# Optimization experiments

Measured on AMD Instinct MI355X. Metric: run time of the kernel, lower is better.

## Reference

```python
import jax, jax.numpy as jnp
import numpy as np

N = 200000
D = 128
B = 8
VS = 0.4
XMIN, YMIN, ZMIN = -50.0, -50.0, -5.0
NX, NY, NZ = 250, 250, 20
VXYZ = NX * NY * NZ
FILL = np.int32(2_000_000_000)  # > any real voxel key, so padded uniques sort last
BN_EPS = 1e-5


def _bn(x, g, b, m, v):
    # BatchNorm1d in eval mode with given running stats
    return (x - m) * jax.lax.rsqrt(v + BN_EPS) * g + b


def _leaky(x):
    return jnp.where(x >= 0, x, 0.1 * x)


def setup_inputs() -> dict:
    key = jax.random.key(0)
    ks = jax.random.split(key, 12)
    points_feature = jax.random.normal(ks[0], (N, D), jnp.float32)
    u = jax.random.uniform(ks[1], (N, 3), jnp.float32)
    lo = jnp.array([XMIN, YMIN, ZMIN], jnp.float32)
    ext = jnp.array([100.0, 100.0, 8.0], jnp.float32)
    points_center = lo + 0.001 + u * (ext - 0.002)  # strictly inside pc_range
    batch_idx = jax.random.randint(ks[2], (N,), 0, B, jnp.int32)
    foreground_mask = jax.random.randint(ks[3], (N,), 0, 2, jnp.int32).astype(bool)
    timestamp = jax.random.normal(ks[4], (B,), jnp.float32) * 0.1
    w_pf = jax.random.normal(ks[5], (3 * D, D), jnp.float32) / np.sqrt(3 * D)
    b_pf = jax.random.normal(ks[6], (D,), jnp.float32) * 0.01
    g_pf = jax.random.uniform(ks[7], (D,), jnp.float32) + 0.5
    be_pf = jax.random.normal(ks[8], (D,), jnp.float32) * 0.1
    m_pf = jax.random.normal(ks[9], (D,), jnp.float32) * 0.1
    v_pf = jax.random.uniform(ks[10], (D,), jnp.float32) + 0.5
    ks2 = jax.random.split(ks[11], 6)
    w_cp = jax.random.normal(ks2[0], (D, D), jnp.float32) / np.sqrt(D)
    b_cp = jax.random.normal(ks2[1], (D,), jnp.float32) * 0.01
    g_cp = jax.random.uniform(ks2[2], (D,), jnp.float32) + 0.5
    be_cp = jax.random.normal(ks2[3], (D,), jnp.float32) * 0.1
    m_cp = jax.random.normal(ks2[4], (D,), jnp.float32) * 0.1
    v_cp = jax.random.uniform(ks2[5], (D,), jnp.float32) + 0.5
    return dict(points_feature=points_feature, points_center=points_center,
                batch_idx=batch_idx, foreground_mask=foreground_mask,
                timestamp=timestamp,
                w_pf=w_pf, b_pf=b_pf, g_pf=g_pf, be_pf=be_pf, m_pf=m_pf, v_pf=v_pf,
                w_cp=w_cp, b_cp=b_cp, g_cp=g_cp, be_cp=be_cp, m_cp=m_cp, v_cp=v_cp)


def reference(points_feature, points_center, batch_idx, foreground_mask, timestamp,
              w_pf, b_pf, g_pf, be_pf, m_pf, v_pf,
              w_cp, b_cp, g_cp, be_cp, m_cp, v_cp):
    # NOTE: the original forward computes a time position embedding and then
    # overwrites it with zeros_like, so its net contribution is exactly zero.
    n = points_feature.shape[0]
    # voxelize point centers -> (b, xi, yi, zi) encoded as a single int key
    xi = jnp.floor((points_center[:, 0] - XMIN) / VS).astype(jnp.int32)
    yi = jnp.floor((points_center[:, 1] - YMIN) / VS).astype(jnp.int32)
    zi = jnp.floor((points_center[:, 2] - ZMIN) / VS).astype(jnp.int32)
    vkey = ((batch_idx.astype(jnp.int32) * NX + xi) * NY + yi) * NZ + zi
    # torch.unique(dim=0) sorts lexicographically == sorted scalar keys
    uk, inv = jnp.unique(vkey, return_inverse=True, size=n, fill_value=FILL)
    fgf = foreground_mask.astype(points_feature.dtype)
    # K = points_cluster_idx_fore.max() + 1 (number of foreground clusters)
    K = jnp.max(jnp.where(foreground_mask, inv, -1)) + 1
    # scatter_mean of foreground point features per cluster (empty -> 0)
    cnt = jax.ops.segment_sum(fgf, inv, num_segments=n)
    csum = jax.ops.segment_sum(points_feature * fgf[:, None], inv, num_segments=n)
    cmean = csum / jnp.maximum(cnt, 1.0)[:, None]
    proj = _leaky(_bn(cmean @ w_cp + b_cp, g_cp, be_cp, m_cp, v_cp))
    valid = jnp.arange(n) < K
    # cluster_feature_all: rows < K hold projected cluster features, rest are 0
    cfa = jnp.where(valid[:, None], proj, 0.0)
    # associate voxels: halve the batch id (agent pairing), re-unique
    akey = (uk // VXYZ // 2) * VXYZ + uk % VXYZ
    _, ainv = jnp.unique(akey, return_inverse=True, size=n, fill_value=FILL)
    # scatter_mean of cluster features over associate voxels (only valid clusters)
    acnt = jax.ops.segment_sum(valid.astype(points_feature.dtype), ainv, num_segments=n)
    asum = jax.ops.segment_sum(cfa, ainv, num_segments=n)
    amean = asum / jnp.maximum(acnt, 1.0)[:, None]
    pf_assoc = amean[ainv[inv]]   # gather per point via voxel -> associate id
    pf_clu = cfa[inv]             # gather per point cluster feature
    amask = (pf_clu - pf_assoc).sum(axis=1) > 0
    cat = jnp.concatenate([points_feature, pf_clu, pf_assoc], axis=1)
    h = _leaky(_bn(cat @ w_pf + b_pf, g_pf, be_pf, m_pf, v_pf))
    newf = jnp.where(amask[:, None], h, points_feature)
    # original early-returns points_feature if associate_mask.sum() <= 1
    return jnp.where(amask.sum() > 1, newf, points_feature)
```

## Files before the change

### kernel.cpp

```cpp
#include <hip/hip_runtime.h>

#define SCAN_BS 256
#define SCAN_IT 16
#define SCAN_CHUNK (SCAN_BS * SCAN_IT)
#define NVOX 10000000
#define NAVOX 5000000
#define NWORDS1 312500
#define NWORDS2 156250
#define VXYZK 1250000

__device__ __forceinline__ float leakyf(float x) { return x >= 0.0f ? x : 0.1f * x; }

__device__ __forceinline__ int fg_get(const void* fgp, int i, int mode) {
  return mode ? (((const unsigned char*)fgp)[i] != 0) : (((const int*)fgp)[i] != 0);
}

__global__ void k_vkey(const float* __restrict__ pc, const int* __restrict__ bidx,
                       const unsigned* __restrict__ fgw, int nw,
                       int* __restrict__ vkey, unsigned* __restrict__ bits,
                       int* __restrict__ c, int N) {
  int i = blockIdx.x * blockDim.x + threadIdx.x;
  if (i < nw && fgw[i] > 1u) atomicOr(&c[4], 1);
  if (i >= N) return;
  float x = pc[3 * i], y = pc[3 * i + 1], z = pc[3 * i + 2];
  int xi = (int)floorf((x - (-50.0f)) / 0.4f);
  int yi = (int)floorf((y - (-50.0f)) / 0.4f);
  int zi = (int)floorf((z - (-5.0f)) / 0.4f);
  xi = min(max(xi, 0), 249); yi = min(max(yi, 0), 249); zi = min(max(zi, 0), 19);
  int b = min(max(bidx[i], 0), 7);
  int key = ((b * 250 + xi) * 250 + yi) * 20 + zi;
  vkey[i] = key;
  atomicOr(&bits[key >> 5], 1u << (key & 31));
}

__global__ void k_scan_pop(const unsigned* __restrict__ bits, int nwords,
                           unsigned* __restrict__ wordpfx, unsigned* __restrict__ bsums) {
  __shared__ unsigned s[SCAN_BS];
  int tid = threadIdx.x;
  long base = (long)blockIdx.x * SCAN_CHUNK + (long)tid * SCAN_IT;
  unsigned v[SCAN_IT];
  unsigned tsum = 0;
#pragma unroll
  for (int j = 0; j < SCAN_IT; ++j) {
    long idx = base + j;
    v[j] = (idx < (long)nwords) ? (unsigned)__popc(bits[idx]) : 0u;
    tsum += v[j];
  }
  unsigned x = tsum;
  s[tid] = x;
  for (int off = 1; off < SCAN_BS; off <<= 1) {
    __syncthreads();
    unsigned y = (tid >= off) ? s[tid - off] : 0u;
    __syncthreads();
    x += y;
    s[tid] = x;
  }
  if (tid == SCAN_BS - 1) bsums[blockIdx.x] = x;
  unsigned run = x - tsum;
#pragma unroll
  for (int j = 0; j < SCAN_IT; ++j) {
    long idx = base + j;
    if (idx < (long)nwords) { wordpfx[idx] = run; run += v[j]; }
  }
}

__global__ void k_scan_sums(unsigned* __restrict__ data, int n, int* __restrict__ totalOut) {
  __shared__ unsigned s[SCAN_BS];
  int tid = threadIdx.x;
  int base = tid * SCAN_IT;
  unsigned v[SCAN_IT];
  unsigned tsum = 0;
#pragma unroll
  for (int j = 0; j < SCAN_IT; ++j) {
    int idx = base + j;
    v[j] = (idx < n) ? data[idx] : 0u;
    tsum += v[j];
  }
  unsigned x = tsum;
  s[tid] = x;
  for (int off = 1; off < SCAN_BS; off <<= 1) {
    __syncthreads();
    unsigned y = (tid >= off) ? s[tid - off] : 0u;
    __syncthreads();
    x += y;
    s[tid] = x;
  }
  if (tid == SCAN_BS - 1) *totalOut = (int)x;
  unsigned run = x - tsum;
#pragma unroll
  for (int j = 0; j < SCAN_IT; ++j) {
    int idx = base + j;
    if (idx < n) { data[idx] = run; run += v[j]; }
  }
}

__device__ __forceinline__ int rank_of(int key, const unsigned* bits,
                                       const unsigned* wordpfx, const unsigned* bsums) {
  int w = key >> 5, b = key & 31;
  return (int)(wordpfx[w] + bsums[w >> 12] + (unsigned)__popc(bits[w] & ((1u << b) - 1u)));
}

__global__ void k_inv_ukey(const int* __restrict__ vkey, const unsigned* __restrict__ bits,
                           const unsigned* __restrict__ wordpfx, const unsigned* __restrict__ bsums,
                           const void* __restrict__ fgp, int* __restrict__ inv,
                           int* __restrict__ ukey, int* __restrict__ c, int N) {
  int i = blockIdx.x * blockDim.x + threadIdx.x;
  bool valid = i < N;
  int mode = c[4];
  int r = 0;
  if (valid) {
    int k = vkey[i];
    r = rank_of(k, bits, wordpfx, bsums);
    inv[i] = r;
    ukey[r] = k;
  }
  int fgr = (valid && fg_get(fgp, i, mode)) ? r : -1;
  for (int off = 32; off > 0; off >>= 1) fgr = max(fgr, __shfl_down(fgr, off));
  if ((threadIdx.x & 63) == 0 && fgr >= 0) atomicMax(&c[2], fgr + 1);
}

__global__ void k_akey_mark(const int* __restrict__ ukey, int* __restrict__ akey,
                            unsigned* __restrict__ abits, const int* __restrict__ c, int N) {
  int r = blockIdx.x * blockDim.x + threadIdx.x;
  if (r >= N || r >= c[0]) return;
  int uk = ukey[r];
  int ak = (uk / VXYZK / 2) * VXYZK + uk % VXYZK;
  akey[r] = ak;
  atomicOr(&abits[ak >> 5], 1u << (ak & 31));
}

__global__ void k_ainv(const int* __restrict__ akey, const unsigned* __restrict__ abits,
                       const unsigned* __restrict__ awordpfx, const unsigned* __restrict__ bsums,
                       int* __restrict__ ainv, unsigned* __restrict__ gcnt,
                       const int* __restrict__ c, int N) {
  int r = blockIdx.x * blockDim.x + threadIdx.x;
  if (r >= N || r >= c[0]) return;
  int g = rank_of(akey[r], abits, awordpfx, bsums);
  ainv[r] = g;
  atomicAdd(&gcnt[g], 1u);
}

__global__ void k_build_lists(const int* __restrict__ ainv_u, const unsigned* __restrict__ gcnt,
                              int* __restrict__ mlist, int* __restrict__ nlist,
                              unsigned char* __restrict__ needp, int* __restrict__ c, int N) {
  int r = blockIdx.x * blockDim.x + threadIdx.x;
  if (r >= N || r >= c[0]) return;
  if (gcnt[ainv_u[r]] >= 2u) {
    int mp = atomicAdd(&c[5], 1);
    mlist[mp] = r;
    if (r < c[2]) {
      needp[r] = 1;
      int np = atomicAdd(&c[6], 1);
      nlist[np] = r;
    }
  }
}

__global__ void k_zero_filter(const int* __restrict__ mlist, const int* __restrict__ ainv_u,
                              const void* __restrict__ fgp, const int* __restrict__ inv,
                              const unsigned char* __restrict__ needp,
                              float* __restrict__ csum, float* __restrict__ asum,
                              float* __restrict__ cnt, int* __restrict__ clist,
                              int* __restrict__ c, int N) {
  int stride = gridDim.x * blockDim.x;
  int tid0 = blockIdx.x * blockDim.x + threadIdx.x;
  int K = c[2];
  int totalA = c[5] * 128;
  for (int idx = tid0; idx < totalA; idx += stride) {
    int r = mlist[idx >> 7];
    int d = idx & 127;
    asum[(size_t)ainv_u[r] * 128 + d] = 0.0f;
    if (r < K) csum[(size_t)r * 128 + d] = 0.0f;
  }
  int mode = c[4];
  for (int i = tid0; i < N; i += stride) {
    if (!fg_get(fgp, i, mode)) continue;
    int r = inv[i];
    if (!needp[r]) continue;
    atomicAdd(&cnt[r], 1.0f);
    int p = atomicAdd(&c[7], 1);
    clist[p] = i;
  }
}

__global__ void k_csum_accum(const float* __restrict__ pf, const int* __restrict__ clist,
                             const int* __restrict__ inv, float* __restrict__ csum,
                             const int* __restrict__ c) {
  int total = c[7] * 128;
  int stride = gridDim.x * blockDim.x;
  for (int idx = blockIdx.x * blockDim.x + threadIdx.x; idx < total; idx += stride) {
    int i = clist[idx >> 7];
    int d = idx & 127;
    atomicAdd(&csum[(size_t)inv[i] * 128 + d], pf[(size_t)i * 128 + d]);
  }
}

__global__ __launch_bounds__(128) void k_proj16(
    float* __restrict__ cs, const float* __restrict__ cnt, const int* __restrict__ nlist,
    const float* __restrict__ W, const float* __restrict__ bb,
    const float* __restrict__ gg, const float* __restrict__ be,
    const float* __restrict__ mm, const float* __restrict__ vv, const int* __restrict__ c) {
  int nc = c[6];
  int ntiles = (nc + 15) >> 4;
  __shared__ __align__(16) float tile[16][128];
  __shared__ int srow[16];
  int d = threadIdx.x;
  for (int tb = blockIdx.x; tb < ntiles; tb += gridDim.x) {
    int base = tb * 16;
    if (d < 16) srow[d] = (base + d < nc) ? nlist[base + d] : -1;
    __syncthreads();
    for (int p = 0; p < 16; ++p) {
      int r = srow[p];
      tile[p][d] = (r >= 0) ? cs[(size_t)r * 128 + d] / fmaxf(cnt[r], 1.0f) : 0.0f;
    }
    __syncthreads();
    float acc[16];
#pragma unroll
    for (int p = 0; p < 16; ++p) acc[p] = 0.0f;
    for (int k4 = 0; k4 < 32; ++k4) {
      float w0 = W[(4 * k4 + 0) * 128 + d];
      float w1 = W[(4 * k4 + 1) * 128 + d];
      float w2 = W[(4 * k4 + 2) * 128 + d];
      float w3 = W[(4 * k4 + 3) * 128 + d];
#pragma unroll
      for (int p = 0; p < 16; ++p) {
        float4 t4 = *(const float4*)&tile[p][4 * k4];
        acc[p] = fmaf(t4.x, w0, acc[p]);
        acc[p] = fmaf(t4.y, w1, acc[p]);
        acc[p] = fmaf(t4.z, w2, acc[p]);
        acc[p] = fmaf(t4.w, w3, acc[p]);
      }
    }
    float biasd = bb[d], scale = gg[d] / sqrtf(vv[d] + 1e-5f), md = mm[d], bed = be[d];
    for (int p = 0; p < 16; ++p) {
      int r = srow[p];
      if (r >= 0) {
        float pre = acc[p] + biasd;
        cs[(size_t)r * 128 + d] = leakyf((pre - md) * scale + bed);
      }
    }
    __syncthreads();
  }
}

__global__ void k_asum_accum(const float* __restrict__ cs, const int* __restrict__ nlist,
                             const int* __restrict__ ainv_u, float* __restrict__ asum,
                             float* __restrict__ acnt, const int* __restrict__ c) {
  int total = c[6] * 128;
  int stride = gridDim.x * blockDim.x;
  for (int idx = blockIdx.x * blockDim.x + threadIdx.x; idx < total; idx += stride) {
    int r = nlist[idx >> 7];
    int d = idx & 127;
    int g = ainv_u[r];
    atomicAdd(&asum[(size_t)g * 128 + d], cs[(size_t)r * 128 + d]);
    if (d == 0) atomicAdd(&acnt[g], 1.0f);
  }
}

__global__ void k_amask2(const float* __restrict__ cs, const float* __restrict__ asum,
                         const float* __restrict__ acnt, const int* __restrict__ ainv_u,
                         const int* __restrict__ mlist, const int* __restrict__ c,
                         unsigned* __restrict__ flag) {
  int mcount = c[5];
  int groups = gridDim.x * (blockDim.x >> 6);
  int j0 = blockIdx.x * (blockDim.x >> 6) + (threadIdx.x >> 6);
  int lane = threadIdx.x & 63;
  int K = c[2];
  for (int j = j0; j < mcount; j += groups) {
    int r = mlist[j];
    int g = ainv_u[r];
    float mc = fmaxf(acnt[g], 1.0f);
    bool valid = r < K;
    size_t rb = (size_t)r * 128, gb = (size_t)g * 128;
    float c0 = valid ? cs[rb + lane] : 0.0f;
    float c1 = valid ? cs[rb + 64 + lane] : 0.0f;
    float s = (c0 - asum[gb + lane] / mc) + (c1 - asum[gb + 64 + lane] / mc);
    for (int off = 32; off > 0; off >>= 1) s += __shfl_down(s, off);
    if (lane == 0) flag[r] = (s > 0.0f) ? 1u : 0u;
  }
}

__global__ void k_plist(const int* __restrict__ inv, const unsigned* __restrict__ flag,
                        int* __restrict__ plist, int* __restrict__ c, int N) {
  int i = blockIdx.x * blockDim.x + threadIdx.x;
  bool pred = (i < N) && (flag[inv[i]] != 0u);
  unsigned long long m = __ballot(pred);
  int lane = threadIdx.x & 63;
  int cnt = __popcll(m);
  int base = 0;
  if (lane == 0 && cnt) base = atomicAdd(&c[3], cnt);
  base = __shfl(base, 0);
  if (pred) plist[base + __popcll(m & ((1ull << lane) - 1ull))] = i;
}

__global__ __launch_bounds__(128) void k_fgemm(
    const float* __restrict__ pf, const float* __restrict__ cs,
    const float* __restrict__ asum, const float* __restrict__ acnt,
    const int* __restrict__ inv, const int* __restrict__ ainv_u,
    const int* __restrict__ plist, const int* __restrict__ c,
    const float* __restrict__ W, const float* __restrict__ bb,
    const float* __restrict__ gg, const float* __restrict__ be,
    const float* __restrict__ mm, const float* __restrict__ vv,
    float* __restrict__ out) {
  int pcnt = c[3];
  if (pcnt <= 1) return;
  int K = c[2];
  int ntiles = (pcnt + 15) >> 4;
  __shared__ __align__(16) float tile[16][384];
  __shared__ int si[16], sr[16], sg[16];
  __shared__ float smc[16];
  int t = threadIdx.x;
  for (int tb = blockIdx.x; tb < ntiles; tb += gridDim.x) {
    int base = tb * 16;
    if (t < 16) {
      int i = (base + t < pcnt) ? plist[base + t] : -1;
      si[t] = i;
      int r = (i >= 0) ? inv[i] : 0;
      sr[t] = r;
      int g = ainv_u[r];
      sg[t] = g;
      smc[t] = fmaxf(acnt[g], 1.0f);
    }
    __syncthreads();
    for (int e = t; e < 16 * 96; e += 128) {
      int p = e / 96, f4 = e % 96;
      int i = si[p];
      float4 v = make_float4(0.f, 0.f, 0.f, 0.f);
      if (i >= 0) {
        if (f4 < 32) {
          v = ((const float4*)pf)[(size_t)i * 32 + f4];
        } else if (f4 < 64) {
          int r = sr[p];
          if (r < K) v = ((const float4*)cs)[(size_t)r * 32 + (f4 - 32)];
        } else {
          float4 a = ((const float4*)asum)[(size_t)sg[p] * 32 + (f4 - 64)];
          float mc = smc[p];
          v = make_float4(a.x / mc, a.y / mc, a.z / mc, a.w / mc);
        }
      }
      *(float4*)&tile[p][f4 * 4] = v;
    }
    __syncthreads();
    float acc[16];
#pragma unroll
    for (int p = 0; p < 16; ++p) acc[p] = 0.0f;
    for (int k4 = 0; k4 < 96; ++k4) {
      float w0 = W[(4 * k4 + 0) * 128 + t];
      float w1 = W[(4 * k4 + 1) * 128 + t];
      float w2 = W[(4 * k4 + 2) * 128 + t];
      float w3 = W[(4 * k4 + 3) * 128 + t];
#pragma unroll
      for (int p = 0; p < 16; ++p) {
        float4 t4 = *(const float4*)&tile[p][4 * k4];
        acc[p] = fmaf(t4.x, w0, acc[p]);
        acc[p] = fmaf(t4.y, w1, acc[p]);
        acc[p] = fmaf(t4.z, w2, acc[p]);
        acc[p] = fmaf(t4.w, w3, acc[p]);
      }
    }
    float biasd = bb[t], scale = gg[t] / sqrtf(vv[t] + 1e-5f), md = mm[t], bed = be[t];
    for (int p = 0; p < 16; ++p) {
      int i = si[p];
      if (i >= 0) {
        float pre = acc[p] + biasd;
        out[(size_t)i * 128 + t] = leakyf((pre - md) * scale + bed);
      }
    }
    __syncthreads();
  }
}

extern "C" void kernel_launch(void* const* d_in, const int* in_sizes, int n_in,
                              void* d_out, int out_size, void* d_ws, size_t ws_size,
                              hipStream_t stream) {
  (void)n_in; (void)out_size; (void)ws_size;
  const float* pf   = (const float*)d_in[0];
  const float* pc   = (const float*)d_in[1];
  const int*   bidx = (const int*)d_in[2];
  const void*  fgp  = d_in[3];
  const float* Wpf  = (const float*)d_in[5];
  const float* bpf  = (const float*)d_in[6];
  const float* gpf  = (const float*)d_in[7];
  const float* bepf = (const float*)d_in[8];
  const float* mpf  = (const float*)d_in[9];
  const float* vpf  = (const float*)d_in[10];
  const float* Wcp  = (const float*)d_in[11];
  const float* bcp  = (const float*)d_in[12];
  const float* gcp  = (const float*)d_in[13];
  const float* becp = (const float*)d_in[14];
  const float* mcp  = (const float*)d_in[15];
  const float* vcp  = (const float*)d_in[16];
  float* out = (float*)d_out;
  int N = in_sizes[0] / 128;

  char* ws = (char*)d_ws;
  size_t o = 0;
  auto take = [&](size_t bytes) -> void* {
    void* p = ws + o;
    o += (bytes + 255) & ~(size_t)255;
    return p;
  };
  unsigned* bits   = (unsigned*)take((size_t)NWORDS1 * 4);
  unsigned* abits  = (unsigned*)take((size_t)NWORDS2 * 4);
  float* cnt       = (float*)take((size_t)N * 4);
  float* acnt      = (float*)take((size_t)N * 4);
  unsigned* flag   = (unsigned*)take((size_t)N * 4);
  unsigned* gcnt   = (unsigned*)take((size_t)N * 4);
  unsigned char* needp = (unsigned char*)take((size_t)N);
  int* ctr         = (int*)take(256);
  size_t zeroBytes = o;
  unsigned* wordpfx  = (unsigned*)take((size_t)NWORDS1 * 4);
  unsigned* awordpfx = (unsigned*)take((size_t)NWORDS2 * 4);
  unsigned* bsums1 = (unsigned*)take((size_t)4096 * 4);
  unsigned* bsums2 = (unsigned*)take((size_t)4096 * 4);
  int* vkey        = (int*)take((size_t)N * 4);
  int* inv         = (int*)take((size_t)N * 4);
  int* ukey        = (int*)take((size_t)N * 4);
  int* akey        = (int*)take((size_t)N * 4);
  int* ainv_u      = (int*)take((size_t)N * 4);
  int* nlist       = (int*)take((size_t)N * 4);
  int* clist       = (int*)take((size_t)N * 4);
  float* csum      = (float*)take((size_t)N * 128 * 4);
  float* asum      = (float*)take((size_t)N * 128 * 4);
  int* mlist = vkey;
  int* plist = akey;

  hipMemcpyAsync(out, pf, (size_t)N * 128 * sizeof(float),
                 hipMemcpyDeviceToDevice, stream);

  hipMemsetAsync(ws, 0, zeroBytes, stream);

  int nb = (N + 255) / 256;
  int nw = N / 4;
  k_vkey<<<nb, 256, 0, stream>>>(pc, bidx, (const unsigned*)fgp, nw, vkey, bits, ctr, N);

  int blk1 = (NWORDS1 + SCAN_CHUNK - 1) / SCAN_CHUNK;
  k_scan_pop<<<blk1, SCAN_BS, 0, stream>>>(bits, NWORDS1, wordpfx, bsums1);
  k_scan_sums<<<1, SCAN_BS, 0, stream>>>(bsums1, blk1, &ctr[0]);
  k_inv_ukey<<<nb, 256, 0, stream>>>(vkey, bits, wordpfx, bsums1, fgp, inv, ukey, ctr, N);

  k_akey_mark<<<nb, 256, 0, stream>>>(ukey, akey, abits, ctr, N);
  int blk2 = (NWORDS2 + SCAN_CHUNK - 1) / SCAN_CHUNK;
  k_scan_pop<<<blk2, SCAN_BS, 0, stream>>>(abits, NWORDS2, awordpfx, bsums2);
  k_scan_sums<<<1, SCAN_BS, 0, stream>>>(bsums2, blk2, &ctr[1]);
  k_ainv<<<nb, 256, 0, stream>>>(akey, abits, awordpfx, bsums2, ainv_u, gcnt, ctr, N);

  k_build_lists<<<nb, 256, 0, stream>>>(ainv_u, gcnt, mlist, nlist, needp, ctr, N);
  k_zero_filter<<<1024, 256, 0, stream>>>(mlist, ainv_u, fgp, inv, needp,
                                          csum, asum, cnt, clist, ctr, N);
  k_csum_accum<<<1024, 256, 0, stream>>>(pf, clist, inv, csum, ctr);
  k_proj16<<<512, 128, 0, stream>>>(csum, cnt, nlist, Wcp, bcp, gcp, becp, mcp, vcp, ctr);
  k_asum_accum<<<512, 256, 0, stream>>>(csum, nlist, ainv_u, asum, acnt, ctr);
  k_amask2<<<512, 256, 0, stream>>>(csum, asum, acnt, ainv_u, mlist, ctr, flag);

  k_plist<<<nb, 256, 0, stream>>>(inv, flag, plist, ctr, N);
  k_fgemm<<<1024, 128, 0, stream>>>(pf, csum, asum, acnt, inv, ainv_u, plist, ctr,
                                    Wpf, bpf, gpf, bepf, mpf, vpf, out);
}
```

Measured before the change: 467.6 us.

## Fuse output copy into voxel-key kernel and merge akey and asum passes

The device-to-device memcpy of the point features into the output moves into the voxel-key kernel as a grid-stride float4 copy. The associate-key marking is folded into the inverse-rank kernel, computed per point rather than per unique voxel, which drops the ukey buffer and one launch. The asum/acnt scatter is fused into the cluster projection epilogue, removing a separate kernel and a re-read of csum. In exchange, the abits atomics now run once per point instead of once per unique voxel, and the output copy no longer uses the copy engine.

```diff
diff --git a/kernel.cpp b/kernel.cpp
--- a/kernel.cpp
+++ b/kernel.cpp
@@ -8,6 +8,8 @@
 #define NWORDS1 312500
 #define NWORDS2 156250
 #define VXYZK 1250000
+#define BLK1 ((NWORDS1 + SCAN_CHUNK - 1) / SCAN_CHUNK)
+#define BLK2 ((NWORDS2 + SCAN_CHUNK - 1) / SCAN_CHUNK)
 
 __device__ __forceinline__ float leakyf(float x) { return x >= 0.0f ? x : 0.1f * x; }
 
@@ -15,22 +17,40 @@
   return mode ? (((const unsigned char*)fgp)[i] != 0) : (((const int*)fgp)[i] != 0);
 }
 
-__global__ void k_vkey(const float* __restrict__ pc, const int* __restrict__ bidx,
-                       const unsigned* __restrict__ fgw, int nw,
-                       int* __restrict__ vkey, unsigned* __restrict__ bits,
-                       int* __restrict__ c, int N) {
-  int i = blockIdx.x * blockDim.x + threadIdx.x;
-  if (i < nw && fgw[i] > 1u) atomicOr(&c[4], 1);
-  if (i >= N) return;
-  float x = pc[3 * i], y = pc[3 * i + 1], z = pc[3 * i + 2];
-  int xi = (int)floorf((x - (-50.0f)) / 0.4f);
-  int yi = (int)floorf((y - (-50.0f)) / 0.4f);
-  int zi = (int)floorf((z - (-5.0f)) / 0.4f);
-  xi = min(max(xi, 0), 249); yi = min(max(yi, 0), 249); zi = min(max(zi, 0), 19);
-  int b = min(max(bidx[i], 0), 7);
-  int key = ((b * 250 + xi) * 250 + yi) * 20 + zi;
-  vkey[i] = key;
-  atomicOr(&bits[key >> 5], 1u << (key & 31));
+__device__ __forceinline__ int rank_of(int key, const unsigned* bits,
+                                       const unsigned* wordpfx, const unsigned* bsums) {
+  int w = key >> 5, b = key & 31;
+  return (int)(wordpfx[w] + bsums[w >> 12] + (unsigned)__popc(bits[w] & ((1u << b) - 1u)));
+}
+
+__global__ void k_vkey_copy(const float* __restrict__ pc, const int* __restrict__ bidx,
+                            const unsigned* __restrict__ fgw, int nw,
+                            int* __restrict__ vkey, unsigned* __restrict__ bits,
+                            int* __restrict__ c, const float* __restrict__ pf,
+                            float* __restrict__ out, int N) {
+  int nth = gridDim.x * blockDim.x;
+  int gtid = blockIdx.x * blockDim.x + threadIdx.x;
+  for (int i = gtid; i < N; i += nth) {
+    if (i < nw && fgw[i] > 1u) atomicOr(&c[4], 1);
+    float x = pc[3 * i], y = pc[3 * i + 1], z = pc[3 * i + 2];
+    int xi = (int)floorf((x - (-50.0f)) / 0.4f);
+    int yi = (int)floorf((y - (-50.0f)) / 0.4f);
+    int zi = (int)floorf((z - (-5.0f)) / 0.4f);
+    xi = min(max(xi, 0), 249); yi = min(max(yi, 0), 249); zi = min(max(zi, 0), 19);
+    int b = min(max(bidx[i], 0), 7);
+    int key = ((b * 250 + xi) * 250 + yi) * 20 + zi;
+    vkey[i] = key;
+    atomicOr(&bits[key >> 5], 1u << (key & 31));
+  }
+  const float4* s4 = (const float4*)pf;
+  float4* d4 = (float4*)out;
+  int n4 = N * 32;
+  int e = gtid;
+  for (; e + 3 * nth < n4; e += 4 * nth) {
+    float4 v0 = s4[e], v1 = s4[e + nth], v2 = s4[e + 2 * nth], v3 = s4[e + 3 * nth];
+    d4[e] = v0; d4[e + nth] = v1; d4[e + 2 * nth] = v2; d4[e + 3 * nth] = v3;
+  }
+  for (; e < n4; e += nth) d4[e] = s4[e];
 }
 
 __global__ void k_scan_pop(const unsigned* __restrict__ bits, int nwords,
@@ -94,16 +114,11 @@
   }
 }
 
-__device__ __forceinline__ int rank_of(int key, const unsigned* bits,
-                                       const unsigned* wordpfx, const unsigned* bsums) {
-  int w = key >> 5, b = key & 31;
-  return (int)(wordpfx[w] + bsums[w >> 12] + (unsigned)__popc(bits[w] & ((1u << b) - 1u)));
-}
-
-__global__ void k_inv_ukey(const int* __restrict__ vkey, const unsigned* __restrict__ bits,
+__global__ void k_inv_akey(const int* __restrict__ vkey, const unsigned* __restrict__ bits,
                            const unsigned* __restrict__ wordpfx, const unsigned* __restrict__ bsums,
                            const void* __restrict__ fgp, int* __restrict__ inv,
-                           int* __restrict__ ukey, int* __restrict__ c, int N) {
+                           int* __restrict__ akey, unsigned* __restrict__ abits,
+                           int* __restrict__ c, int N) {
   int i = blockIdx.x * blockDim.x + threadIdx.x;
   bool valid = i < N;
   int mode = c[4];
@@ -112,21 +127,13 @@
     int k = vkey[i];
     r = rank_of(k, bits, wordpfx, bsums);
     inv[i] = r;
-    ukey[r] = k;
+    int ak = (k / VXYZK / 2) * VXYZK + k % VXYZK;
+    akey[r] = ak;
+    atomicOr(&abits[ak >> 5], 1u << (ak & 31));
   }
   int fgr = (valid && fg_get(fgp, i, mode)) ? r : -1;
   for (int off = 32; off > 0; off >>= 1) fgr = max(fgr, __shfl_down(fgr, off));
   if ((threadIdx.x & 63) == 0 && fgr >= 0) atomicMax(&c[2], fgr + 1);
-}
-
-__global__ void k_akey_mark(const int* __restrict__ ukey, int* __restrict__ akey,
-                            unsigned* __restrict__ abits, const int* __restrict__ c, int N) {
-  int r = blockIdx.x * blockDim.x + threadIdx.x;
-  if (r >= N || r >= c[0]) return;
-  int uk = ukey[r];
-  int ak = (uk / VXYZK / 2) * VXYZK + uk % VXYZK;
-  akey[r] = ak;
-  atomicOr(&abits[ak >> 5], 1u << (ak & 31));
 }
 
 __global__ void k_ainv(const int* __restrict__ akey, const unsigned* __restrict__ abits,
@@ -195,8 +202,9 @@
   }
 }
 
-__global__ __launch_bounds__(128) void k_proj16(
+__global__ __launch_bounds__(128) void k_proj_asum(
     float* __restrict__ cs, const float* __restrict__ cnt, const int* __restrict__ nlist,
+    const int* __restrict__ ainv_u, float* __restrict__ asum, float* __restrict__ acnt,
     const float* __restrict__ W, const float* __restrict__ bb,
     const float* __restrict__ gg, const float* __restrict__ be,
     const float* __restrict__ mm, const float* __restrict__ vv, const int* __restrict__ c) {
@@ -236,24 +244,14 @@
       int r = srow[p];
       if (r >= 0) {
         float pre = acc[p] + biasd;
-        cs[(size_t)r * 128 + d] = leakyf((pre - md) * scale + bed);
+        float val = leakyf((pre - md) * scale + bed);
+        cs[(size_t)r * 128 + d] = val;
+        int g = ainv_u[r];
+        atomicAdd(&asum[(size_t)g * 128 + d], val);
+        if (d == 0) atomicAdd(&acnt[g], 1.0f);
       }
     }
     __syncthreads();
-  }
-}
-
-__global__ void k_asum_accum(const float* __restrict__ cs, const int* __restrict__ nlist,
-                             const int* __restrict__ ainv_u, float* __restrict__ asum,
-                             float* __restrict__ acnt, const int* __restrict__ c) {
-  int total = c[6] * 128;
-  int stride = gridDim.x * blockDim.x;
-  for (int idx = blockIdx.x * blockDim.x + threadIdx.x; idx < total; idx += stride) {
-    int r = nlist[idx >> 7];
-    int d = idx & 127;
-    int g = ainv_u[r];
-    atomicAdd(&asum[(size_t)g * 128 + d], cs[(size_t)r * 128 + d]);
-    if (d == 0) atomicAdd(&acnt[g], 1.0f);
   }
 }
 
@@ -415,7 +413,6 @@
   unsigned* bsums2 = (unsigned*)take((size_t)4096 * 4);
   int* vkey        = (int*)take((size_t)N * 4);
   int* inv         = (int*)take((size_t)N * 4);
-  int* ukey        = (int*)take((size_t)N * 4);
   int* akey        = (int*)take((size_t)N * 4);
   int* ainv_u      = (int*)take((size_t)N * 4);
   int* nlist       = (int*)take((size_t)N * 4);
@@ -425,32 +422,28 @@
   int* mlist = vkey;
   int* plist = akey;
 
-  hipMemcpyAsync(out, pf, (size_t)N * 128 * sizeof(float),
-                 hipMemcpyDeviceToDevice, stream);
-
   hipMemsetAsync(ws, 0, zeroBytes, stream);
 
   int nb = (N + 255) / 256;
   int nw = N / 4;
-  k_vkey<<<nb, 256, 0, stream>>>(pc, bidx, (const unsigned*)fgp, nw, vkey, bits, ctr, N);
-
-  int blk1 = (NWORDS1 + SCAN_CHUNK - 1) / SCAN_CHUNK;
-  k_scan_pop<<<blk1, SCAN_BS, 0, stream>>>(bits, NWORDS1, wordpfx, bsums1);
-  k_scan_sums<<<1, SCAN_BS, 0, stream>>>(bsums1, blk1, &ctr[0]);
-  k_inv_ukey<<<nb, 256, 0, stream>>>(vkey, bits, wordpfx, bsums1, fgp, inv, ukey, ctr, N);
-
-  k_akey_mark<<<nb, 256, 0, stream>>>(ukey, akey, abits, ctr, N);
-  int blk2 = (NWORDS2 + SCAN_CHUNK - 1) / SCAN_CHUNK;
-  k_scan_pop<<<blk2, SCAN_BS, 0, stream>>>(abits, NWORDS2, awordpfx, bsums2);
-  k_scan_sums<<<1, SCAN_BS, 0, stream>>>(bsums2, blk2, &ctr[1]);
+  k_vkey_copy<<<2048, 256, 0, stream>>>(pc, bidx, (const unsigned*)fgp, nw, vkey, bits,
+                                        ctr, pf, out, N);
+
+  k_scan_pop<<<BLK1, SCAN_BS, 0, stream>>>(bits, NWORDS1, wordpfx, bsums1);
+  k_scan_sums<<<1, SCAN_BS, 0, stream>>>(bsums1, BLK1, &ctr[0]);
+  k_inv_akey<<<nb, 256, 0, stream>>>(vkey, bits, wordpfx, bsums1, fgp, inv,
+                                     akey, abits, ctr, N);
+
+  k_scan_pop<<<BLK2, SCAN_BS, 0, stream>>>(abits, NWORDS2, awordpfx, bsums2);
+  k_scan_sums<<<1, SCAN_BS, 0, stream>>>(bsums2, BLK2, &ctr[1]);
   k_ainv<<<nb, 256, 0, stream>>>(akey, abits, awordpfx, bsums2, ainv_u, gcnt, ctr, N);
 
   k_build_lists<<<nb, 256, 0, stream>>>(ainv_u, gcnt, mlist, nlist, needp, ctr, N);
   k_zero_filter<<<1024, 256, 0, stream>>>(mlist, ainv_u, fgp, inv, needp,
                                           csum, asum, cnt, clist, ctr, N);
   k_csum_accum<<<1024, 256, 0, stream>>>(pf, clist, inv, csum, ctr);
-  k_proj16<<<512, 128, 0, stream>>>(csum, cnt, nlist, Wcp, bcp, gcp, becp, mcp, vcp, ctr);
-  k_asum_accum<<<512, 256, 0, stream>>>(csum, nlist, ainv_u, asum, acnt, ctr);
+  k_proj_asum<<<512, 128, 0, stream>>>(csum, cnt, nlist, ainv_u, asum, acnt,
+                                       Wcp, bcp, gcp, becp, mcp, vcp, ctr);
   k_amask2<<<512, 256, 0, stream>>>(csum, asum, acnt, ainv_u, mlist, ctr, flag);
 
   k_plist<<<nb, 256, 0, stream>>>(inv, flag, plist, ctr, N);
```

Measured after the change: 467.4 us. About the same (-0.0%).
